# Kernel optimization log

Measured on AMD Instinct MI355X. Metric: run time of the kernel, lower is better.

## Reference

```python
import jax, jax.numpy as jnp
import numpy as np
from jax import lax


def _c1x1(t, w, b=None):
    # t: [B,C,H,W], w: [O,C] (1x1 conv == channel matmul)
    y = jnp.einsum('bchw,oc->bohw', t, w)
    if b is not None:
        y = y + b[None, :, None, None]
    return y


def _mamba(u, in_w, conv_w, conv_b, xproj_w, dt_w, dt_b, A_log, Dp, out_w):
    # u: [B,L,d_model]; Mamba block (mamba_ssm defaults: in/out/x_proj bias=False)
    B, L, _ = u.shape
    d_inner = conv_w.shape[0]
    d_state = A_log.shape[1]
    dt_rank = dt_w.shape[1]
    d_conv = conv_w.shape[2]
    xz = jnp.einsum('bld,ed->ble', u, in_w)          # [B,L,2*d_inner]
    xc, z = xz[..., :d_inner], xz[..., d_inner:]
    # depthwise causal conv1d over seq
    xt = jnp.pad(xc.transpose(0, 2, 1), ((0, 0), (0, 0), (d_conv - 1, 0)))
    xt = lax.conv_general_dilated(xt, conv_w, (1,), 'VALID',
                                  feature_group_count=d_inner,
                                  dimension_numbers=('NCH', 'OIH', 'NCH'))
    xc = jax.nn.silu(xt + conv_b[None, :, None]).transpose(0, 2, 1)  # [B,L,d_inner]
    dbc = jnp.einsum('bld,ed->ble', xc, xproj_w)     # [B,L,dt_rank+2*d_state]
    dt = dbc[..., :dt_rank]
    B_ = dbc[..., dt_rank:dt_rank + d_state]
    C_ = dbc[..., dt_rank + d_state:]
    delta = jax.nn.softplus(jnp.einsum('blr,dr->bld', dt, dt_w) + dt_b)  # [B,L,d_inner]
    A = -jnp.exp(A_log)                              # [d_inner,d_state]
    dA = jnp.exp(delta[..., None] * A)               # [B,L,D,N]
    dBu = delta[..., None] * B_[:, :, None, :] * xc[..., None]
    def step(h, inp):
        dA_t, dBu_t, c_t = inp
        h = dA_t * h + dBu_t                         # [B,D,N]
        y = jnp.einsum('bdn,bn->bd', h, c_t)
        return h, y
    h0 = jnp.zeros((B, d_inner, d_state), dtype=u.dtype)
    _, ys = lax.scan(step, h0, (dA.transpose(1, 0, 2, 3),
                                dBu.transpose(1, 0, 2, 3),
                                C_.transpose(1, 0, 2)))
    y = ys.transpose(1, 0, 2) + xc * Dp              # [B,L,d_inner]
    y = y * jax.nn.silu(z)
    return jnp.einsum('bld,od->blo', y, out_w)       # [B,L,d_model]


def setup_inputs() -> dict:
    key = jax.random.key(0)
    B, C, H, W = 8, 128, 160, 160
    mip, d_in, d_st, d_r, d_cv = 8, 256, 16, 8, 4
    ks = iter(jax.random.split(key, 64))
    def rn(shape, s=0.05):
        return (jax.random.normal(next(ks), shape, dtype=jnp.float32) * s)
    inp = {'x': jax.random.normal(next(ks), (B, C, H, W), dtype=jnp.float32)}
    inp.update(conv1_w=rn((mip, C)), conv1_b=rn((mip,)),
               bn_g=jnp.ones((mip,)), bn_b=jnp.zeros((mip,)),
               bn_m=jnp.zeros((mip,)), bn_v=jnp.ones((mip,)),
               convh_w=rn((C, mip)), convh_b=rn((C,)),
               convw_w=rn((C, mip)), convw_b=rn((C,)),
               mlpx_w1=rn((C, C)), mlpx_b1=rn((C,)), mlpx_w2=rn((C, C)), mlpx_b2=rn((C,)),
               mlpy_w1=rn((C, C)), mlpy_b1=rn((C,)), mlpy_w2=rn((C, C)), mlpy_b2=rn((C,)),
               adjust_w=rn((C, 2 * C)))
    for p in ('mx', 'my'):
        inp[p + '_in_w'] = rn((2 * d_in, C))
        inp[p + '_conv_w'] = rn((d_in, 1, d_cv), 0.3)
        inp[p + '_conv_b'] = rn((d_in,))
        inp[p + '_xproj_w'] = rn((d_r + 2 * d_st, d_in))
        inp[p + '_dt_w'] = rn((d_in, d_r))
        inp[p + '_dt_b'] = rn((d_in,))
        inp[p + '_Alog'] = jnp.log(jnp.broadcast_to(jnp.arange(1, d_st + 1, dtype=jnp.float32), (d_in, d_st)))
        inp[p + '_D'] = jnp.ones((d_in,))
        inp[p + '_out_w'] = rn((C, d_in))
    return inp


def reference(x, conv1_w, conv1_b, bn_g, bn_b, bn_m, bn_v, convh_w, convh_b,
              convw_w, convw_b, mlpx_w1, mlpx_b1, mlpx_w2, mlpx_b2,
              mlpy_w1, mlpy_b1, mlpy_w2, mlpy_b2, adjust_w,
              mx_in_w, mx_conv_w, mx_conv_b, mx_xproj_w, mx_dt_w, mx_dt_b,
              mx_Alog, mx_D, mx_out_w,
              my_in_w, my_conv_w, my_conv_b, my_xproj_w, my_dt_w, my_dt_b,
              my_Alog, my_D, my_out_w):
    B, C, H, W = x.shape
    gelu = lambda t: jax.nn.gelu(t, approximate=False)
    # CoordAttWithMLP
    x_h = x.mean(3, keepdims=True)                      # [B,C,H,1]
    x_w = x.mean(2, keepdims=True).transpose(0, 1, 3, 2)  # [B,C,W,1]
    y = jnp.concatenate([x_h, x_w], axis=2)             # [B,C,H+W,1]
    y = _c1x1(y, conv1_w, conv1_b)
    y = (y - bn_m[None, :, None, None]) * jax.lax.rsqrt(bn_v + 1e-5)[None, :, None, None]
    y = y * bn_g[None, :, None, None] + bn_b[None, :, None, None]
    y = gelu(y)
    a_h = _c1x1(y[:, :, :H], convh_w, convh_b)          # [B,C,H,1] (pre-sigmoid)
    a_w = _c1x1(y[:, :, H:].transpose(0, 1, 3, 2), convw_w, convw_b)  # [B,C,1,W]
    # EfficientMambaAttention00
    ux = x.mean(3).transpose(0, 2, 1)                   # [B,H,C]
    x_x = _mamba(ux, mx_in_w, mx_conv_w, mx_conv_b, mx_xproj_w,
                 mx_dt_w, mx_dt_b, mx_Alog, mx_D, mx_out_w)
    x_x = x_x.transpose(0, 2, 1)[..., None]             # [B,C,H,1]
    x_x = jax.nn.sigmoid(x_x + a_h)
    x_x = _c1x1(gelu(_c1x1(x_x, mlpx_w1, mlpx_b1)), mlpx_w2, mlpx_b2)
    uy = x.mean(2).transpose(0, 2, 1)                   # [B,W,C]
    x_y = _mamba(uy, my_in_w, my_conv_w, my_conv_b, my_xproj_w,
                 my_dt_w, my_dt_b, my_Alog, my_D, my_out_w)
    x_y = x_y.transpose(0, 2, 1)[:, :, None, :]         # [B,C,1,W]
    x_y = jax.nn.sigmoid(x_y + a_w)
    x_y = _c1x1(gelu(_c1x1(x_y, mlpy_w1, mlpy_b1)), mlpy_w2, mlpy_b2)
    # combine
    result_h = jax.nn.sigmoid(a_h) * x_y                # [B,C,H,W]
    result_w = jax.nn.sigmoid(a_w) * x_x                # [B,C,H,W]
    out1 = _c1x1(jnp.concatenate([result_h, result_w], axis=1), adjust_w)
    return x * out1
```

## Files before the change

kernel.cpp:

```cpp
#include <hip/hip_runtime.h>
#include <hip/hip_bf16.h>
#include <math.h>


typedef __attribute__((ext_vector_type(8))) short short8;
typedef __attribute__((ext_vector_type(4))) float f32x4;

#define LDS_BARRIER() do { asm volatile("s_waitcnt lgkmcnt(0)" ::: "memory"); \
                           __builtin_amdgcn_s_barrier(); } while(0)

__device__ __forceinline__ float sigm_(float x){ return 1.f/(1.f+__expf(-x)); }
__device__ __forceinline__ float silu_(float x){ return x/(1.f+__expf(-x)); }
__device__ __forceinline__ float gelu_(float x){ return 0.5f*x*(1.f+erff(x*0.7071067811865476f)); }
__device__ __forceinline__ float softplus_(float x){ return (x>20.f)?x:log1pf(__expf(x)); }

__global__ void k_means(const float* __restrict__ x, float* __restrict__ xh, float* __restrict__ xw){
  int bc = blockIdx.x;
  const float* xt = x + (size_t)bc*25600;
  int tid = threadIdx.x, wave = tid>>6, lane = tid&63;
  __shared__ float4 colpart[4][40];
  float csx=0.f, csy=0.f, csz=0.f, csw=0.f;
  for (int i=0;i<40;i++){
    int h = wave*40+i;
    float4 v = make_float4(0.f,0.f,0.f,0.f);
    if (lane<40) v = ((const float4*)(xt + h*160))[lane];
    csx+=v.x; csy+=v.y; csz+=v.z; csw+=v.w;
    float r = v.x+v.y+v.z+v.w;
    for (int off=32; off>0; off>>=1) r += __shfl_down(r, off, 64);
    if (lane==0) xh[(size_t)bc*160+h] = r*(1.f/160.f);
  }
  if (lane<40) colpart[wave][lane] = make_float4(csx,csy,csz,csw);
  __syncthreads();
  if (tid<40){
    float4 a=colpart[0][tid], b=colpart[1][tid], c=colpart[2][tid], d=colpart[3][tid];
    float4 s = make_float4((a.x+b.x+c.x+d.x)*(1.f/160.f), (a.y+b.y+c.y+d.y)*(1.f/160.f),
                           (a.z+b.z+c.z+d.z)*(1.f/160.f), (a.w+b.w+c.w+d.w)*(1.f/160.f));
    ((float4*)(xw + (size_t)bc*160))[tid] = s;
  }
}

__global__ void k_ybranch(const float* __restrict__ xh, const float* __restrict__ xw,
                          const float* __restrict__ w1, const float* __restrict__ b1,
                          const float* __restrict__ bg, const float* __restrict__ bb,
                          const float* __restrict__ bm, const float* __restrict__ bv,
                          float* __restrict__ ybuf){
  int gid = blockIdx.x*blockDim.x + threadIdx.x;
  if (gid >= 8*320) return;
  int b = gid/320, p = gid%320;
  const float* in = (p<160) ? (xh + (size_t)b*128*160 + p) : (xw + (size_t)b*128*160 + (p-160));
  float acc[8] = {0,0,0,0,0,0,0,0};
  for (int c=0;c<128;c++){
    float u = in[c*160];
    #pragma unroll
    for (int m=0;m<8;m++) acc[m] += w1[m*128+c]*u;
  }
  #pragma unroll
  for (int m=0;m<8;m++){
    float val = acc[m] + b1[m];
    val = (val - bm[m]) * rsqrtf(bv[m] + 1e-5f);
    val = val * bg[m] + bb[m];
    ybuf[(b*320+p)*8+m] = gelu_(val);
  }
}

__global__ void k_ahw(const float* __restrict__ ybuf,
                      const float* __restrict__ wh, const float* __restrict__ bh,
                      const float* __restrict__ ww, const float* __restrict__ bw,
                      float* __restrict__ a_h, float* __restrict__ a_w,
                      float* __restrict__ SHT, float* __restrict__ SW,
                      const float* __restrict__ adjw, __hip_bfloat16* __restrict__ adjwb){
  int blk = blockIdx.x;
  if (blk >= 1280){
    int i = (blk-1280)*256 + threadIdx.x;
    if (i < 32768) adjwb[i] = __float2bfloat16(adjw[i]);
    return;
  }
  int gid = blk*256 + threadIdx.x;
  int p = gid%320; int c = (gid/320)%128; int b = gid/(320*128);
  const float* yv = ybuf + (size_t)(b*320+p)*8;
  const float* w = (p<160)? (wh + c*8) : (ww + c*8);
  float acc = (p<160)? bh[c] : bw[c];
  #pragma unroll
  for (int m=0;m<8;m++) acc += w[m]*yv[m];
  if (p<160){
    size_t o = ((size_t)(b*128+c))*160+p;
    a_h[o] = acc;
    SHT[((size_t)(b*160+p))*128 + c] = sigm_(acc);
  } else {
    size_t o = ((size_t)(b*128+c))*160+(p-160);
    a_w[o] = acc; SW[o] = sigm_(acc);
  }
}

__global__ __launch_bounds__(256) void k_inproj(
                         const float* __restrict__ xh, const float* __restrict__ xw,
                         const float* __restrict__ inw0, const float* __restrict__ inw1,
                         float* __restrict__ xcpre, float* __restrict__ zb){
  __shared__ float uS[8][128];
  int blk = blockIdx.x;
  int g = blk/160, rem = blk%160, b = rem/20, lt = rem%20, lbase = lt*8;
  int t = threadIdx.x;
  const float* src = (g==0)? xh : xw;
  {
    int c = t>>1, lh = t&1;
    float4 v = *(const float4*)(src + ((size_t)(b*128+c))*160 + lbase + lh*4);
    uS[lh*4+0][c]=v.x; uS[lh*4+1][c]=v.y; uS[lh*4+2][c]=v.z; uS[lh*4+3][c]=v.w;
  }
  __syncthreads();
  const float* inw = (g==0)? inw0 : inw1;
  const float* w0p = inw + (size_t)t*128;
  const float* w1p = inw + (size_t)(t+256)*128;
  float acc0[8]={0,0,0,0,0,0,0,0}, acc1[8]={0,0,0,0,0,0,0,0};
  for (int ct=0; ct<16; ct++){
    float4 wa = *(const float4*)(w0p + ct*8);
    float4 wb = *(const float4*)(w0p + ct*8 + 4);
    float4 wc = *(const float4*)(w1p + ct*8);
    float4 wd = *(const float4*)(w1p + ct*8 + 4);
    #pragma unroll
    for (int l=0;l<8;l++){
      float4 ua = *(const float4*)&uS[l][ct*8];
      float4 ub = *(const float4*)&uS[l][ct*8+4];
      acc0[l] += wa.x*ua.x + wa.y*ua.y + wa.z*ua.z + wa.w*ua.w
               + wb.x*ub.x + wb.y*ub.y + wb.z*ub.z + wb.w*ub.w;
      acc1[l] += wc.x*ua.x + wc.y*ua.y + wc.z*ua.z + wc.w*ua.w
               + wd.x*ub.x + wd.y*ub.y + wd.z*ub.z + wd.w*ub.w;
    }
  }
  size_t ob = ((size_t)(g*8+b)*160 + lbase)*256;
  #pragma unroll
  for (int l=0;l<8;l++){
    xcpre[ob + (size_t)l*256 + t] = acc0[l];
    zb   [ob + (size_t)l*256 + t] = acc1[l];
  }
}

__global__ void k_conv(const float* __restrict__ xcpre,
                       const float* __restrict__ cw0, const float* __restrict__ cb0,
                       const float* __restrict__ cw1, const float* __restrict__ cb1,
                       float* __restrict__ xcb){
  int gid = blockIdx.x*blockDim.x + threadIdx.x;
  if (gid >= 2*8*160*256) return;
  int d = gid & 255; int t = gid >> 8; int l = t % 160; int gb = t / 160; int g = gb >> 3;
  const float* cw = ((g==0)? cw0 : cw1) + d*4;
  float acc = ((g==0)? cb0 : cb1)[d];
  const float* base = xcpre + (size_t)gb*160*256 + d;
  #pragma unroll
  for (int k=0;k<4;k++){
    int ls = l-3+k;
    if (ls>=0) acc += cw[k] * base[(size_t)ls*256];
  }
  xcb[gid] = silu_(acc);
}

__global__ __launch_bounds__(256) void k_xproj(
                        const float* __restrict__ xcb,
                        const float* __restrict__ xp0, const float* __restrict__ xp1,
                        float* __restrict__ dbc){
  __shared__ float xv[32][260];
  int blk = blockIdx.x;
  int g = blk/40, rem = blk%40, b = rem/5, lt = rem%5, lbase = lt*32;
  int t = threadIdx.x;
  size_t base = ((size_t)(g*8+b)*160 + lbase)*256;
  for (int i=t; i<8192; i+=256){ int l=i>>8, d=i&255; xv[l][d] = xcb[base+i]; }
  __syncthreads();
  int l = t>>3, s = t&7;
  const float* xp = (g==0)? xp0 : xp1;
  size_t orow = ((size_t)(g*8+b)*160 + lbase + l)*40;
  for (int q=0;q<5;q++){
    int j = s + q*8;
    const float* w = xp + j*256;
    float acc=0.f;
    for (int dd=0; dd<256; dd+=8){
      float4 wa = *(const float4*)(w+dd);
      float4 wb = *(const float4*)(w+dd+4);
      float4 ua = *(const float4*)&xv[l][dd];
      float4 ub = *(const float4*)&xv[l][dd+4];
      acc += wa.x*ua.x + wa.y*ua.y + wa.z*ua.z + wa.w*ua.w
           + wb.x*ub.x + wb.y*ub.y + wb.z*ub.z + wb.w*ub.w;
    }
    dbc[orow + j] = acc;
  }
}

__global__ __launch_bounds__(256) void k_scan(
                       const float* __restrict__ dbc,
                       const float* __restrict__ xcb, const float* __restrict__ zb,
                       const float* __restrict__ dtw0, const float* __restrict__ dtb0,
                       const float* __restrict__ dtw1, const float* __restrict__ dtb1,
                       const float* __restrict__ Alog0, const float* __restrict__ Alog1,
                       const float* __restrict__ D0, const float* __restrict__ D1,
                       float* __restrict__ ysb){
  __shared__ float dsS[160][16];
  __shared__ float BS [160][16];
  __shared__ float CS [160][16];
  __shared__ float xcS[160][16];
  __shared__ float yS [160][16];
  int blk = blockIdx.x;
  int gb = blk >> 4, dblk = blk & 15, g = gb >> 3;
  int dbase = dblk*16;
  int t = threadIdx.x;
  size_t base = (size_t)gb*160*256;
  const float* db = dbc + (size_t)gb*6400;
  const float* dtwG = (g==0)? dtw0 : dtw1;
  const float* dtbG = (g==0)? dtb0 : dtb1;

  #pragma unroll
  for (int i=0;i<10;i++){
    int item = t + 256*i;
    int l = item>>4, c = item&15;
    const float* r = db + l*40;
    int d = dbase + c;
    const float* wt = dtwG + d*8;
    float4 w0 = *(const float4*)wt;
    float4 w1 = *(const float4*)(wt+4);
    float4 r0 = *(const float4*)r;
    float4 r1 = *(const float4*)(r+4);
    float dt = dtbG[d] + w0.x*r0.x+w0.y*r0.y+w0.z*r0.z+w0.w*r0.w
                       + w1.x*r1.x+w1.y*r1.y+w1.z*r1.z+w1.w*r1.w;
    dsS[l][c] = softplus_(dt);
    BS [l][c] = r[8+c];
    CS [l][c] = r[24+c];
    xcS[l][c] = xcb[base + (size_t)l*256 + dbase + c];
  }
  __syncthreads();

  int dloc = t>>4, n = t&15;
  int d = dbase + dloc;
  float A  = -__expf(((g==0)? Alog0 : Alog1)[d*16+n]);
  float Dd = ((g==0)? D0 : D1)[d];
  float h = 0.f;
  for (int lc=0; lc<160; lc+=8){
    float ds8[8], B8[8], C8[8], xc8[8];
    #pragma unroll
    for (int j=0;j<8;j++){
      ds8[j]=dsS[lc+j][dloc]; B8[j]=BS[lc+j][n];
      C8[j]=CS[lc+j][n];      xc8[j]=xcS[lc+j][dloc];
    }
    #pragma unroll
    for (int j=0;j<8;j++){
      float dA = __expf(ds8[j]*A);
      h = dA*h + ds8[j]*B8[j]*xc8[j];
      float p = h*C8[j];
      p += __shfl_xor(p,1,16); p += __shfl_xor(p,2,16);
      p += __shfl_xor(p,4,16); p += __shfl_xor(p,8,16);
      if (n==0) yS[lc+j][dloc] = p + xc8[j]*Dd;
    }
  }
  __syncthreads();

  #pragma unroll
  for (int i=0;i<10;i++){
    int item = t + 256*i;
    int l = item>>4, c = item&15;
    size_t gi = base + (size_t)l*256 + dbase + c;
    ysb[gi] = yS[l][c] * silu_(zb[gi]);
  }
}

__global__ __launch_bounds__(256) void k_post(
                       const float* __restrict__ ysb,
                       const float* __restrict__ ow0, const float* __restrict__ ow1,
                       const float* __restrict__ a_h, const float* __restrict__ a_w,
                       const float* __restrict__ w1x, const float* __restrict__ b1x,
                       const float* __restrict__ w1y, const float* __restrict__ b1y,
                       const float* __restrict__ w2x, const float* __restrict__ b2x,
                       const float* __restrict__ w2y, const float* __restrict__ b2y,
                       float* __restrict__ QxT, float* __restrict__ Qy){
  __shared__ float ysS[10][256];
  __shared__ float Sc[10][128];
  __shared__ float Sp[10][128];
  int blk = blockIdx.x;
  int g = blk>>7, rem = blk&127, b = rem>>4, lt = rem&15, lbase = lt*10;
  int t = threadIdx.x; int c = t&127, kh = t>>7;
  size_t ybase = ((size_t)(g*8+b)*160 + lbase)*256;
  for (int i=t; i<2560; i+=256) ((float*)ysS)[i] = ysb[ybase+i];
  __syncthreads();
  float acc[10];
  {
    const float* w = ((g==0)? ow0 : ow1) + (size_t)c*256 + kh*128;
    #pragma unroll
    for (int l=0;l<10;l++) acc[l]=0.f;
    for (int ct=0; ct<16; ct++){
      float4 wa = *(const float4*)(w + ct*8);
      float4 wb = *(const float4*)(w + ct*8 + 4);
      #pragma unroll
      for (int l=0;l<10;l++){
        float4 ua = *(const float4*)&ysS[l][kh*128+ct*8];
        float4 ub = *(const float4*)&ysS[l][kh*128+ct*8+4];
        acc[l] += wa.x*ua.x + wa.y*ua.y + wa.z*ua.z + wa.w*ua.w
                + wb.x*ub.x + wb.y*ub.y + wb.z*ub.z + wb.w*ub.w;
      }
    }
  }
  if (kh==1){ for (int l=0;l<10;l++) Sc[l][c] = acc[l]; }
  __syncthreads();
  if (kh==0){
    const float* a = ((g==0)? a_h : a_w) + ((size_t)(b*128+c))*160 + lbase;
    #pragma unroll
    for (int l=0;l<10;l++) Sp[l][c] = sigm_(acc[l] + Sc[l][c] + a[l]);
  }
  __syncthreads();
  {
    const float* w = ((g==0)? w1x : w1y) + (size_t)c*128 + kh*64;
    #pragma unroll
    for (int l=0;l<10;l++) acc[l]=0.f;
    for (int ct=0; ct<8; ct++){
      float4 wa = *(const float4*)(w + ct*8);
      float4 wb = *(const float4*)(w + ct*8 + 4);
      #pragma unroll
      for (int l=0;l<10;l++){
        float4 ua = *(const float4*)&Sp[l][kh*64+ct*8];
        float4 ub = *(const float4*)&Sp[l][kh*64+ct*8+4];
        acc[l] += wa.x*ua.x + wa.y*ua.y + wa.z*ua.z + wa.w*ua.w
                + wb.x*ub.x + wb.y*ub.y + wb.z*ub.z + wb.w*ub.w;
      }
    }
  }
  if (kh==1){ for (int l=0;l<10;l++) Sc[l][c] = acc[l]; }
  __syncthreads();
  if (kh==0){
    float bb = ((g==0)? b1x : b1y)[c];
    float tv[10];
    #pragma unroll
    for (int l=0;l<10;l++) tv[l] = gelu_(bb + acc[l] + Sc[l][c]);
    __syncthreads();
    #pragma unroll
    for (int l=0;l<10;l++) Sp[l][c] = tv[l];
  } else {
    __syncthreads();
  }
  __syncthreads();
  {
    const float* w = ((g==0)? w2x : w2y) + (size_t)c*128 + kh*64;
    #pragma unroll
    for (int l=0;l<10;l++) acc[l]=0.f;
    for (int ct=0; ct<8; ct++){
      float4 wa = *(const float4*)(w + ct*8);
      float4 wb = *(const float4*)(w + ct*8 + 4);
      #pragma unroll
      for (int l=0;l<10;l++){
        float4 ua = *(const float4*)&Sp[l][kh*64+ct*8];
        float4 ub = *(const float4*)&Sp[l][kh*64+ct*8+4];
        acc[l] += wa.x*ua.x + wa.y*ua.y + wa.z*ua.z + wa.w*ua.w
                + wb.x*ub.x + wb.y*ub.y + wb.z*ub.z + wb.w*ub.w;
      }
    }
  }
  if (kh==1){ for (int l=0;l<10;l++) Sc[l][c] = acc[l]; }
  __syncthreads();
  if (kh==0){
    float bb = ((g==0)? b2x : b2y)[c];
    if (g==0){
      #pragma unroll
      for (int l=0;l<10;l++)
        QxT[((size_t)(b*160 + lbase + l))*128 + c] = bb + acc[l] + Sc[l][c];
    } else {
      size_t orow = ((size_t)(b*128+c))*160 + lbase;
      #pragma unroll
      for (int l=0;l<10;l++) Qy[orow + l] = bb + acc[l] + Sc[l][c];
    }
  }
}

__device__ __forceinline__ void build_F(__hip_bfloat16* Fb, float s, const float4* v,
                                        int wg, int kq){
  #pragma unroll
  for (int u=0;u<4;u++){
    int wr = wg*16 + u*4;
    Fb[(wr+0)*136 + kq] = __float2bfloat16(s*v[u].x);
    Fb[(wr+1)*136 + kq] = __float2bfloat16(s*v[u].y);
    Fb[(wr+2)*136 + kq] = __float2bfloat16(s*v[u].z);
    Fb[(wr+3)*136 + kq] = __float2bfloat16(s*v[u].w);
  }
}

__global__ __launch_bounds__(256,4) void k_final_mfma(
                       const float* __restrict__ x,
                       const float* __restrict__ SHT, const float* __restrict__ SW,
                       const float* __restrict__ QxT, const float* __restrict__ Qy,
                       const __hip_bfloat16* __restrict__ adjwb, float* __restrict__ out){
  __shared__ __hip_bfloat16 F[2][32*136];
  int blk0 = blockIdx.x;
  int b = blk0 & 7, inner = blk0 >> 3;
  int ht = inner/5, wq = inner%5;
  int h0 = ht*5;
  int wbase = wq*32;
  int tid = threadIdx.x;
  int kq = tid & 127, wg = tid >> 7;
  int wid = tid>>6, lane = tid&63, quad = lane>>4, l16 = lane&15;

  float s0[5], s1[5];
  #pragma unroll
  for (int j=0;j<5;j++){
    s0[j] = SHT[((size_t)(b*160+h0+j))*128 + kq];
    s1[j] = QxT[((size_t)(b*160+h0+j))*128 + kq];
  }
  size_t prow = ((size_t)(b*128+kq))*160 + wbase + wg*16;
  const float4* rp0 = (const float4*)(Qy + prow);
  const float4* rp1 = (const float4*)(SW + prow);
  float4 v0[4], v1[4];
  #pragma unroll
  for (int u=0;u<4;u++) v0[u] = rp0[u];
  #pragma unroll
  for (int u=0;u<4;u++) v1[u] = rp1[u];

  build_F(F[0], s0[0], v0, wg, kq);
  LDS_BARRIER();

  size_t rowA = ((size_t)(b*128 + wid*32 + l16))*25600 + wbase + quad*4;
  size_t rowB = rowA + (size_t)16*25600;

  #pragma unroll
  for (int j=0;j<5;j++){
    int h = h0 + j;
    float4 xv[2][2];
    #pragma unroll
    for (int nt=0;nt<2;nt++){
      xv[0][nt] = *(const float4*)(x + rowA + (size_t)h*160 + nt*16);
      xv[1][nt] = *(const float4*)(x + rowB + (size_t)h*160 + nt*16);
    }
    f32x4 acc[2][2];
    #pragma unroll
    for (int i=0;i<2;i++)
      #pragma unroll
      for (int nt=0;nt<2;nt++) acc[i][nt] = (f32x4){0.f,0.f,0.f,0.f};

    {
      short8 bf[2][4];
      #pragma unroll
      for (int i=0;i<2;i++){
        const __hip_bfloat16* bp = adjwb + (size_t)(wid*32 + i*16 + l16)*256 + quad*8;
        #pragma unroll
        for (int kc=0;kc<4;kc++) bf[i][kc] = *(const short8*)(bp + kc*32);
      }
      #pragma unroll
      for (int nt=0; nt<2; nt++){
        const __hip_bfloat16* ap = &F[0][(nt*16 + l16)*136 + quad*8];
        #pragma unroll
        for (int kc=0;kc<4;kc++){
          short8 af = *(const short8*)(ap + kc*32);
          acc[0][nt] = __builtin_amdgcn_mfma_f32_16x16x32_bf16(af, bf[0][kc], acc[0][nt], 0,0,0);
          acc[1][nt] = __builtin_amdgcn_mfma_f32_16x16x32_bf16(af, bf[1][kc], acc[1][nt], 0,0,0);
        }
      }
    }
    build_F(F[1], s1[j], v1, wg, kq);
    LDS_BARRIER();

    {
      short8 bf[2][4];
      #pragma unroll
      for (int i=0;i<2;i++){
        const __hip_bfloat16* bp = adjwb + (size_t)(wid*32 + i*16 + l16)*256 + 128 + quad*8;
        #pragma unroll
        for (int kc=0;kc<4;kc++) bf[i][kc] = *(const short8*)(bp + kc*32);
      }
      #pragma unroll
      for (int nt=0; nt<2; nt++){
        const __hip_bfloat16* ap = &F[1][(nt*16 + l16)*136 + quad*8];
        #pragma unroll
        for (int kc=0;kc<4;kc++){
          short8 af = *(const short8*)(ap + kc*32);
          acc[0][nt] = __builtin_amdgcn_mfma_f32_16x16x32_bf16(af, bf[0][kc], acc[0][nt], 0,0,0);
          acc[1][nt] = __builtin_amdgcn_mfma_f32_16x16x32_bf16(af, bf[1][kc], acc[1][nt], 0,0,0);
        }
      }
    }
    if (j<4) build_F(F[0], s0[j+1], v0, wg, kq);

    #pragma unroll
    for (int i=0;i<2;i++){
      size_t rb = (i? rowB : rowA) + (size_t)h*160;
      #pragma unroll
      for (int nt=0; nt<2; nt++){
        f32x4 a = acc[i][nt];
        float4 xvv = xv[i][nt];
        float4 ov = make_float4(xvv.x*a[0], xvv.y*a[1], xvv.z*a[2], xvv.w*a[3]);
        *(float4*)(out + rb + nt*16) = ov;
      }
    }
    LDS_BARRIER();
  }
}

extern "C" void kernel_launch(void* const* d_in, const int* in_sizes, int n_in,
                              void* d_out, int out_size, void* d_ws, size_t ws_size,
                              hipStream_t stream) {
  #define W(i) ((const float*)d_in[i])
  const float* X = W(0);
  float* ws = (float*)d_ws;
  float* xh    = ws;
  float* xw    = xh    + 163840;
  float* ybuf  = xw    + 163840;
  float* ah    = ybuf  + 20480;
  float* aw    = ah    + 163840;
  float* xcpre = aw    + 163840;
  float* zb    = xcpre + 655360;
  float* xcb   = zb    + 655360;
  float* dbc   = xcb   + 655360;
  float* ysb   = dbc   + 102400;
  float* QxT   = ysb   + 655360;
  float* Qy    = QxT   + 163840;
  __hip_bfloat16* adjwb = (__hip_bfloat16*)xcpre;
  float* SHT   = xcpre + 16384;
  float* SW    = SHT   + 163840;

  k_means  <<<1024, 256, 0, stream>>>(X, xh, xw);
  k_ybranch<<<10,   256, 0, stream>>>(xh, xw, W(1), W(2), W(3), W(4), W(5), W(6), ybuf);
  k_inproj <<<320,  256, 0, stream>>>(xh, xw, W(20), W(29), xcpre, zb);
  k_conv   <<<2560, 256, 0, stream>>>(xcpre, W(21), W(22), W(30), W(31), xcb);
  k_ahw    <<<1408, 256, 0, stream>>>(ybuf, W(7), W(8), W(9), W(10), ah, aw, SHT, SW,
                                      W(19), adjwb);
  k_xproj  <<<80,   256, 0, stream>>>(xcb, W(23), W(32), dbc);
  k_scan   <<<256,  256, 0, stream>>>(dbc, xcb, zb, W(24), W(25), W(33), W(34),
                                      W(26), W(35), W(27), W(36), ysb);
  k_post   <<<256,  256, 0, stream>>>(ysb, W(28), W(37), ah, aw,
                                      W(11), W(12), W(15), W(16),
                                      W(13), W(14), W(17), W(18), QxT, Qy);
  k_final_mfma<<<1280, 256, 0, stream>>>(X, SHT, SW, QxT, Qy, adjwb, (float*)d_out);
  #undef W
}
```

Before: 463.9 us.

## Fuse y-branch into a_h/a_w kernel, rework mean reduction, split xproj finer

Merges the y-branch conv/BN/GELU kernel into the a_h/a_w kernel. Each block now stages eight positions of pooled input in shared memory and computes the 8-channel intermediate cooperatively instead of using a 10-block kernel, which removes one launch and the ybuf round trip. The means kernel now builds row sums through a shared-memory partial table instead of a wave shuffle per row. The x_proj kernel is split into twice as many blocks with smaller tiles to raise parallelism, at the cost of some idle threads in the last output pass.

After: 423.4 us. 8.7% less time.

```diff
diff --git a/kernel.cpp b/kernel.cpp
--- a/kernel.cpp
+++ b/kernel.cpp
@@ -14,24 +14,32 @@
 __device__ __forceinline__ float gelu_(float x){ return 0.5f*x*(1.f+erff(x*0.7071067811865476f)); }
 __device__ __forceinline__ float softplus_(float x){ return (x>20.f)?x:log1pf(__expf(x)); }
 
-__global__ void k_means(const float* __restrict__ x, float* __restrict__ xh, float* __restrict__ xw){
+__global__ __launch_bounds__(256) void k_means(const float* __restrict__ x,
+                                               float* __restrict__ xh, float* __restrict__ xw){
   int bc = blockIdx.x;
   const float* xt = x + (size_t)bc*25600;
   int tid = threadIdx.x, wave = tid>>6, lane = tid&63;
+  __shared__ float part[160][41];
   __shared__ float4 colpart[4][40];
-  float csx=0.f, csy=0.f, csz=0.f, csw=0.f;
-  for (int i=0;i<40;i++){
-    int h = wave*40+i;
-    float4 v = make_float4(0.f,0.f,0.f,0.f);
-    if (lane<40) v = ((const float4*)(xt + h*160))[lane];
-    csx+=v.x; csy+=v.y; csz+=v.z; csw+=v.w;
-    float r = v.x+v.y+v.z+v.w;
-    for (int off=32; off>0; off>>=1) r += __shfl_down(r, off, 64);
-    if (lane==0) xh[(size_t)bc*160+h] = r*(1.f/160.f);
-  }
-  if (lane<40) colpart[wave][lane] = make_float4(csx,csy,csz,csw);
-  __syncthreads();
-  if (tid<40){
+  if (lane < 40){
+    float csx=0.f, csy=0.f, csz=0.f, csw=0.f;
+    #pragma unroll 4
+    for (int i=0;i<40;i++){
+      int r = wave*40+i;
+      float4 v = ((const float4*)(xt + r*160))[lane];
+      csx+=v.x; csy+=v.y; csz+=v.z; csw+=v.w;
+      part[r][lane] = (v.x+v.y)+(v.z+v.w);
+    }
+    colpart[wave][lane] = make_float4(csx,csy,csz,csw);
+  }
+  __syncthreads();
+  if (tid < 160){
+    float s = 0.f;
+    #pragma unroll
+    for (int k=0;k<40;k++) s += part[tid][k];
+    xh[(size_t)bc*160 + tid] = s*(1.f/160.f);
+  }
+  if (tid < 40){
     float4 a=colpart[0][tid], b=colpart[1][tid], c=colpart[2][tid], d=colpart[3][tid];
     float4 s = make_float4((a.x+b.x+c.x+d.x)*(1.f/160.f), (a.y+b.y+c.y+d.y)*(1.f/160.f),
                            (a.z+b.z+c.z+d.z)*(1.f/160.f), (a.w+b.w+c.w+d.w)*(1.f/160.f));
@@ -39,56 +47,86 @@
   }
 }
 
-__global__ void k_ybranch(const float* __restrict__ xh, const float* __restrict__ xw,
-                          const float* __restrict__ w1, const float* __restrict__ b1,
-                          const float* __restrict__ bg, const float* __restrict__ bb,
-                          const float* __restrict__ bm, const float* __restrict__ bv,
-                          float* __restrict__ ybuf){
-  int gid = blockIdx.x*blockDim.x + threadIdx.x;
-  if (gid >= 8*320) return;
-  int b = gid/320, p = gid%320;
-  const float* in = (p<160) ? (xh + (size_t)b*128*160 + p) : (xw + (size_t)b*128*160 + (p-160));
-  float acc[8] = {0,0,0,0,0,0,0,0};
-  for (int c=0;c<128;c++){
-    float u = in[c*160];
-    #pragma unroll
-    for (int m=0;m<8;m++) acc[m] += w1[m*128+c]*u;
-  }
-  #pragma unroll
-  for (int m=0;m<8;m++){
-    float val = acc[m] + b1[m];
-    val = (val - bm[m]) * rsqrtf(bv[m] + 1e-5f);
-    val = val * bg[m] + bb[m];
-    ybuf[(b*320+p)*8+m] = gelu_(val);
-  }
-}
-
-__global__ void k_ahw(const float* __restrict__ ybuf,
+__global__ __launch_bounds__(256) void k_yahw(
+                      const float* __restrict__ xh, const float* __restrict__ xw,
+                      const float* __restrict__ w1, const float* __restrict__ b1,
+                      const float* __restrict__ bg, const float* __restrict__ bb,
+                      const float* __restrict__ bm, const float* __restrict__ bv,
                       const float* __restrict__ wh, const float* __restrict__ bh,
                       const float* __restrict__ ww, const float* __restrict__ bw,
                       float* __restrict__ a_h, float* __restrict__ a_w,
                       float* __restrict__ SHT, float* __restrict__ SW,
                       const float* __restrict__ adjw, __hip_bfloat16* __restrict__ adjwb){
   int blk = blockIdx.x;
-  if (blk >= 1280){
-    int i = (blk-1280)*256 + threadIdx.x;
+  int t = threadIdx.x;
+  if (blk >= 320){
+    int i = (blk-320)*256 + t;
     if (i < 32768) adjwb[i] = __float2bfloat16(adjw[i]);
     return;
   }
-  int gid = blk*256 + threadIdx.x;
-  int p = gid%320; int c = (gid/320)%128; int b = gid/(320*128);
-  const float* yv = ybuf + (size_t)(b*320+p)*8;
-  const float* w = (p<160)? (wh + c*8) : (ww + c*8);
-  float acc = (p<160)? bh[c] : bw[c];
-  #pragma unroll
-  for (int m=0;m<8;m++) acc += w[m]*yv[m];
-  if (p<160){
-    size_t o = ((size_t)(b*128+c))*160+p;
-    a_h[o] = acc;
-    SHT[((size_t)(b*160+p))*128 + c] = sigm_(acc);
-  } else {
-    size_t o = ((size_t)(b*128+c))*160+(p-160);
-    a_w[o] = acc; SW[o] = sigm_(acc);
+  __shared__ float xS[8][128];
+  __shared__ float ppart[256];
+  __shared__ float yS[8][9];
+  int b = blk/40, pt = blk%40;
+  int p0 = pt*8;
+  bool isH = (pt < 20);
+  const float* src = isH ? xh : xw;
+  int pp0 = isH ? p0 : (p0-160);
+  {
+    int c = t>>1, h2 = t&1;
+    float4 v = *(const float4*)(src + ((size_t)(b*128+c))*160 + pp0 + h2*4);
+    xS[h2*4+0][c]=v.x; xS[h2*4+1][c]=v.y; xS[h2*4+2][c]=v.z; xS[h2*4+3][c]=v.w;
+  }
+  __syncthreads();
+  {
+    int p8 = t>>5, m = (t>>2)&7, q = t&3;
+    const float* wrow = w1 + m*128 + q*32;
+    const float* xrow = &xS[p8][q*32];
+    float acc = 0.f;
+    #pragma unroll
+    for (int k4=0;k4<8;k4++){
+      float4 wv = *(const float4*)(wrow + k4*4);
+      float4 uv = *(const float4*)(xrow + k4*4);
+      acc += wv.x*uv.x + wv.y*uv.y + wv.z*uv.z + wv.w*uv.w;
+    }
+    ppart[t] = acc;
+  }
+  __syncthreads();
+  if (t < 64){
+    int p8 = t>>3, m = t&7;
+    float val = b1[m] + ppart[t*4+0] + ppart[t*4+1] + ppart[t*4+2] + ppart[t*4+3];
+    val = (val - bm[m]) * rsqrtf(bv[m] + 1e-5f);
+    val = val * bg[m] + bb[m];
+    yS[p8][m] = gelu_(val);
+  }
+  __syncthreads();
+  {
+    int c = t&127, pg = t>>7;
+    const float* wrow2 = (isH ? wh : ww) + c*8;
+    float wreg[8];
+    #pragma unroll
+    for (int m=0;m<8;m++) wreg[m] = wrow2[m];
+    float bias = (isH ? bh : bw)[c];
+    float accp[4];
+    #pragma unroll
+    for (int j=0;j<4;j++){
+      int p = pg*4 + j;
+      float a = bias;
+      #pragma unroll
+      for (int m=0;m<8;m++) a += wreg[m]*yS[p][m];
+      accp[j] = a;
+    }
+    size_t rowo = ((size_t)(b*128+c))*160 + pp0 + pg*4;
+    if (isH){
+      *(float4*)(a_h + rowo) = make_float4(accp[0],accp[1],accp[2],accp[3]);
+      #pragma unroll
+      for (int j=0;j<4;j++)
+        SHT[((size_t)(b*160 + p0 + pg*4 + j))*128 + c] = sigm_(accp[j]);
+    } else {
+      *(float4*)(a_w + rowo) = make_float4(accp[0],accp[1],accp[2],accp[3]);
+      *(float4*)(SW + rowo) = make_float4(sigm_(accp[0]),sigm_(accp[1]),
+                                          sigm_(accp[2]),sigm_(accp[3]));
+    }
   }
 }
 
@@ -156,18 +194,19 @@
                         const float* __restrict__ xcb,
                         const float* __restrict__ xp0, const float* __restrict__ xp1,
                         float* __restrict__ dbc){
-  __shared__ float xv[32][260];
+  __shared__ float xv[16][260];
   int blk = blockIdx.x;
-  int g = blk/40, rem = blk%40, b = rem/5, lt = rem%5, lbase = lt*32;
+  int g = blk/80, rem = blk%80, b = rem/10, lt = rem%10, lbase = lt*16;
   int t = threadIdx.x;
   size_t base = ((size_t)(g*8+b)*160 + lbase)*256;
-  for (int i=t; i<8192; i+=256){ int l=i>>8, d=i&255; xv[l][d] = xcb[base+i]; }
-  __syncthreads();
-  int l = t>>3, s = t&7;
+  for (int i=t; i<4096; i+=256){ int l=i>>8, d=i&255; xv[l][d] = xcb[base+i]; }
+  __syncthreads();
+  int l = t>>4, s = t&15;
   const float* xp = (g==0)? xp0 : xp1;
   size_t orow = ((size_t)(g*8+b)*160 + lbase + l)*40;
-  for (int q=0;q<5;q++){
-    int j = s + q*8;
+  for (int q=0;q<3;q++){
+    int j = s + q*16;
+    if (j >= 40) break;
     const float* w = xp + j*256;
     float acc=0.f;
     for (int dd=0; dd<256; dd+=8){
@@ -506,12 +545,12 @@
   float* SW    = SHT   + 163840;
 
   k_means  <<<1024, 256, 0, stream>>>(X, xh, xw);
-  k_ybranch<<<10,   256, 0, stream>>>(xh, xw, W(1), W(2), W(3), W(4), W(5), W(6), ybuf);
   k_inproj <<<320,  256, 0, stream>>>(xh, xw, W(20), W(29), xcpre, zb);
   k_conv   <<<2560, 256, 0, stream>>>(xcpre, W(21), W(22), W(30), W(31), xcb);
-  k_ahw    <<<1408, 256, 0, stream>>>(ybuf, W(7), W(8), W(9), W(10), ah, aw, SHT, SW,
+  k_yahw   <<<448,  256, 0, stream>>>(xh, xw, W(1), W(2), W(3), W(4), W(5), W(6),
+                                      W(7), W(8), W(9), W(10), ah, aw, SHT, SW,
                                       W(19), adjwb);
-  k_xproj  <<<80,   256, 0, stream>>>(xcb, W(23), W(32), dbc);
+  k_xproj  <<<160,  256, 0, stream>>>(xcb, W(23), W(32), dbc);
   k_scan   <<<256,  256, 0, stream>>>(dbc, xcb, zb, W(24), W(25), W(33), W(34),
                                       W(26), W(35), W(27), W(36), ysb);
   k_post   <<<256,  256, 0, stream>>>(ysb, W(28), W(37), ah, aw,
```
